# Optimization experiments

Measured on AMD Instinct MI355X. Metric: run time of the kernel, lower is better.

The kernel has to match this reference:

```python
import math
import jax, jax.numpy as jnp
import numpy as np

B, Q, K, D = 32, 1024, 1024, 128
MASK_VALUE = -1000000.0


def setup_inputs() -> dict:
    key = jax.random.key(0)
    kq, kk, kv, kl = jax.random.split(key, 4)
    return {
        "queries": jax.random.normal(kq, (B, Q, D), dtype=jnp.float32),
        "keys": jax.random.normal(kk, (B, K, D), dtype=jnp.float32),
        "values": jax.random.normal(kv, (B, K, D), dtype=jnp.float32),
        "valid_lens": jax.random.randint(kl, (B,), 1, K + 1, dtype=jnp.int32),
    }


def reference(queries, keys, values, valid_lens):
    d = queries.shape[-1]
    # scores: [B, Q, K]
    scores = jnp.einsum("bqd,bkd->bqk", queries, keys) / math.sqrt(d)
    # key-padding mask: position k valid iff k < valid_lens[b] (broadcast over queries)
    mask = jnp.arange(keys.shape[1])[None, None, :] < valid_lens[:, None, None]
    scores = jnp.where(mask, scores, MASK_VALUE)
    attn = jax.nn.softmax(scores, axis=-1)
    # dropout p=0.0 -> identity
    return jnp.einsum("bqk,bkv->bqv", attn, values)
```

## Files before the change

kernel.cpp:

```cpp
#include <hip/hip_runtime.h>
#include <math.h>

typedef _Float16 f16;
typedef __attribute__((ext_vector_type(8))) _Float16 f16x8;
typedef __attribute__((ext_vector_type(4))) _Float16 f16x4;
typedef __attribute__((ext_vector_type(4))) float f32x4;

constexpr int BATCH = 32;
constexpr int QL = 1024;
constexpr int KL = 1024;
constexpr int D = 128;
constexpr int BQ = 64;
constexpr int BK = 64;
constexpr int CT = 8;
constexpr int DKP = 136;
constexpr int BKP = 72;

#define CSC 0.12752863187087177f

static __device__ __forceinline__ f16x4 pk4(float x, float y, float z, float w) {
  auto a = __builtin_amdgcn_cvt_pkrtz(x, y);
  auto b = __builtin_amdgcn_cvt_pkrtz(z, w);
  f16x4 h;
  h[0] = (f16)a[0]; h[1] = (f16)a[1]; h[2] = (f16)b[0]; h[3] = (f16)b[1];
  return h;
}
static __device__ __forceinline__ f16x8 pk8(float4 u, float4 v) {
  f16x4 a = pk4(u.x, u.y, u.z, u.w);
  f16x4 b = pk4(v.x, v.y, v.z, v.w);
  f16x8 h;
  h[0] = a[0]; h[1] = a[1]; h[2] = a[2]; h[3] = a[3];
  h[4] = b[0]; h[5] = b[1]; h[6] = b[2]; h[7] = b[3];
  return h;
}
static __device__ __forceinline__ f16x8 pk8v(f32x4 a, f32x4 b) {
  auto x0 = __builtin_amdgcn_cvt_pkrtz(a[0], a[1]);
  auto x1 = __builtin_amdgcn_cvt_pkrtz(a[2], a[3]);
  auto x2 = __builtin_amdgcn_cvt_pkrtz(b[0], b[1]);
  auto x3 = __builtin_amdgcn_cvt_pkrtz(b[2], b[3]);
  f16x8 h;
  h[0] = x0[0]; h[1] = x0[1]; h[2] = x1[0]; h[3] = x1[1];
  h[4] = x2[0]; h[5] = x2[1]; h[6] = x3[0]; h[7] = x3[1];
  return h;
}
static __device__ __forceinline__ f16x8 pk8s(float4 u, float4 v) {
  float4 a = {u.x * CSC, u.y * CSC, u.z * CSC, u.w * CSC};
  float4 b = {v.x * CSC, v.y * CSC, v.z * CSC, v.w * CSC};
  return pk8(a, b);
}

static __device__ __forceinline__ int krp(int kk) {
  return ((kk >> 5) << 5) | (((kk >> 2) & 1) << 4) | (((kk >> 3) & 3) << 2) | (kk & 3);
}

#define ISSUE(KR, VR, T)                                                   \
  do {                                                                     \
    const float4* Kt = (const float4*)(Kb + (size_t)(T) * BK * D);         \
    _Pragma("unroll")                                                      \
    for (int i_ = 0; i_ < 4; ++i_) {                                       \
      int cc_ = tid + i_ * 256;                                            \
      int row_ = cc_ >> 4, d04_ = (cc_ & 15) * 2;                          \
      KR[2 * i_]     = Kt[row_ * 32 + d04_];                               \
      KR[2 * i_ + 1] = Kt[row_ * 32 + d04_ + 1];                           \
    }                                                                      \
    const float* Vt = Vb + (size_t)(T) * BK * D;                           \
    _Pragma("unroll")                                                      \
    for (int i_ = 0; i_ < 2; ++i_) {                                       \
      int f_ = tid + i_ * 256;                                             \
      const float* base_ = Vt + (size_t)((f_ & 15) * 4) * D + (f_ >> 4) * 4; \
      VR[i_ * 4 + 0] = *(const float4*)(base_);                            \
      VR[i_ * 4 + 1] = *(const float4*)(base_ + D);                        \
      VR[i_ * 4 + 2] = *(const float4*)(base_ + 2 * D);                    \
      VR[i_ * 4 + 3] = *(const float4*)(base_ + 3 * D);                    \
    }                                                                      \
  } while (0)

#define DRAIN(KR, VR, NB)                                                  \
  do {                                                                     \
    _Pragma("unroll")                                                      \
    for (int i_ = 0; i_ < 4; ++i_) {                                       \
      int cc_ = tid + i_ * 256;                                            \
      int row_ = cc_ >> 4, d0_ = (cc_ & 15) * 8;                           \
      *(f16x8*)&sK[NB][krp(row_)][d0_] = pk8(KR[2 * i_], KR[2 * i_ + 1]);  \
    }                                                                      \
    _Pragma("unroll")                                                      \
    for (int i_ = 0; i_ < 2; ++i_) {                                       \
      int f_ = tid + i_ * 256;                                             \
      int k0_ = (f_ & 15) * 4, d0_ = (f_ >> 4) * 4;                        \
      float4 r0_ = VR[i_*4+0], r1_ = VR[i_*4+1], r2_ = VR[i_*4+2], r3_ = VR[i_*4+3]; \
      *(f16x4*)&sVT[NB][d0_ + 0][k0_] = pk4(r0_.x, r1_.x, r2_.x, r3_.x);   \
      *(f16x4*)&sVT[NB][d0_ + 1][k0_] = pk4(r0_.y, r1_.y, r2_.y, r3_.y);   \
      *(f16x4*)&sVT[NB][d0_ + 2][k0_] = pk4(r0_.z, r1_.z, r2_.z, r3_.z);   \
      *(f16x4*)&sVT[NB][d0_ + 3][k0_] = pk4(r0_.w, r1_.w, r2_.w, r3_.w);   \
    }                                                                      \
  } while (0)

#define TILE_BARRIER()                                                     \
  do {                                                                     \
    asm volatile("s_waitcnt lgkmcnt(0)" ::: "memory");                     \
    __builtin_amdgcn_s_barrier();                                          \
    asm volatile("" ::: "memory");                                         \
  } while (0)

__global__ __launch_bounds__(256, 2)
void attn_fwd(const float* __restrict__ Qp, const float* __restrict__ Kp,
              const float* __restrict__ Vp, const int* __restrict__ VLp,
              float* __restrict__ Op, float* __restrict__ wsO,
              float* __restrict__ wsL, int nks) {
  __shared__ f16 sK[2][BK][DKP];
  __shared__ f16 sVT[2][D][BKP];
  __shared__ int sN[32];
  __shared__ int sI[32];

  const int tid  = threadIdx.x;
  const int wave = tid >> 6, lane = tid & 63;
  const int l16  = lane & 15, quad = lane >> 4;

  if (tid < 32) sN[tid] = (VLp[tid] + BK - 1) / BK;
  __syncthreads();
  if (tid < 32) {
    int nb = sN[tid], r = 0;
    #pragma unroll
    for (int k = 0; k < 32; ++k) {
      int nk = sN[k];
      r += (nk > nb) || (nk == nb && k < tid);
    }
    sI[r] = tid;
  }
  __syncthreads();

  const int xcd = blockIdx.x & 7;
  const int j   = (int)blockIdx.x >> 3;

  int b, qt, ks, t0, t1, nt, vl;
  if (nks == 2) {
    ks = j >> 6;
    const int lb = (j >> 4) & 3;
    qt = j & 15;
    const int gr = (lb == 0) ? xcd : (lb == 1) ? (15 - xcd)
                 : (lb == 2) ? (16 + xcd) : (31 - xcd);
    b  = sI[gr];
    vl = VLp[b];
    nt = (vl + BK - 1) / BK;
    t0 = ks * CT;
    t1 = min(nt, t0 + CT);
    if (t0 >= t1) return;
  } else {
    const int jj = (j < 32) ? j : (95 - j);
    const int lr = jj >> 4;
    qt = jj & 15;
    ks = 0;
    const int gr = (lr == 0) ? xcd : (lr == 1) ? (15 - xcd)
                 : (lr == 2) ? (16 + xcd) : (31 - xcd);
    b  = sI[gr];
    vl = VLp[b];
    nt = (vl + BK - 1) / BK;
    t0 = 0; t1 = nt;
  }

  const float* Kb = Kp + (size_t)b * KL * D;
  const float* Vb = Vp + (size_t)b * KL * D;

  float4 kreg[8], vreg[8];

  const float* Qb = Qp + ((size_t)(b * QL + qt * BQ + wave * 16 + l16)) * D;
  float4 qtmp[8];
  #pragma unroll
  for (int kc = 0; kc < 4; ++kc) {
    const float* p = Qb + kc * 32 + quad * 8;
    qtmp[2 * kc]     = *(const float4*)p;
    qtmp[2 * kc + 1] = *(const float4*)(p + 4);
  }

  ISSUE(kreg, vreg, t0);

  f16x8 qf[4];
  #pragma unroll
  for (int kc = 0; kc < 4; ++kc) qf[kc] = pk8s(qtmp[2 * kc], qtmp[2 * kc + 1]);

  float lsum = 0.f;
  f32x4 o[8];
  #pragma unroll
  for (int dt = 0; dt < 8; ++dt) o[dt] = (f32x4){0.f, 0.f, 0.f, 0.f};

  DRAIN(kreg, vreg, 0);
  TILE_BARRIER();

  for (int t = t0; t < t1; ++t) {
    const int cur = (t - t0) & 1, nxt = cur ^ 1;
    const bool more = (t + 1 < t1);

    if (more) ISSUE(kreg, vreg, t + 1);

    f32x4 sv[4];
    #pragma unroll
    for (int ct = 0; ct < 4; ++ct) {
      f32x4 cacc = (f32x4){0.f, 0.f, 0.f, 0.f};
      #pragma unroll
      for (int kc = 0; kc < 4; ++kc) {
        f16x8 kf = *(const f16x8*)&sK[cur][ct * 16 + l16][kc * 32 + quad * 8];
        cacc = __builtin_amdgcn_mfma_f32_16x16x32_f16(kf, qf[kc], cacc, 0, 0, 0);
      }
      sv[ct] = cacc;
    }

    if (t * BK + BK > vl) {
      #pragma unroll
      for (int ct = 0; ct < 4; ++ct) {
        int kb = t * BK + (ct >> 1) * 32 + (ct & 1) * 4 + quad * 8;
        #pragma unroll
        for (int r = 0; r < 4; ++r)
          sv[ct][r] = (kb + r) < vl ? sv[ct][r] : -1.0e9f;
      }
    }

    #pragma unroll
    for (int ct = 0; ct < 4; ++ct) {
      #pragma unroll
      for (int r = 0; r < 4; ++r) {
        float p = __builtin_amdgcn_exp2f(sv[ct][r]);
        sv[ct][r] = p;
        lsum += p;
      }
    }
    f16x8 pf0 = pk8v(sv[0], sv[1]);
    f16x8 pf1 = pk8v(sv[2], sv[3]);

    #pragma unroll
    for (int dt = 0; dt < 8; ++dt) {
      f16x8 vf0 = *(const f16x8*)&sVT[cur][dt * 16 + l16][quad * 8];
      o[dt] = __builtin_amdgcn_mfma_f32_16x16x32_f16(vf0, pf0, o[dt], 0, 0, 0);
      f16x8 vf1 = *(const f16x8*)&sVT[cur][dt * 16 + l16][32 + quad * 8];
      o[dt] = __builtin_amdgcn_mfma_f32_16x16x32_f16(vf1, pf1, o[dt], 0, 0, 0);
    }

    if (more) DRAIN(kreg, vreg, nxt);
    TILE_BARRIER();
  }

  float ls = lsum;
  ls += __shfl_xor(ls, 16);
  ls += __shfl_xor(ls, 32);

  if (nks == 1 || nt <= CT) {
    float* Ob = Op + ((size_t)(b * QL + qt * BQ + wave * 16)) * D;
    const float inv = 1.0f / ls;
    #pragma unroll
    for (int dt = 0; dt < 8; ++dt) {
      float4 w = {o[dt][0] * inv, o[dt][1] * inv, o[dt][2] * inv, o[dt][3] * inv};
      *(float4*)&Ob[(size_t)l16 * D + dt * 16 + quad * 4] = w;
    }
  } else {
    const int pair = b * 16 + qt;
    float* dst = (ks == 0)
        ? Op + ((size_t)(b * QL + qt * BQ + wave * 16)) * D
        : wsO + (size_t)pair * BQ * D + (size_t)(wave * 16) * D;
    #pragma unroll
    for (int dt = 0; dt < 8; ++dt) {
      float4 w = {o[dt][0], o[dt][1], o[dt][2], o[dt][3]};
      *(float4*)&dst[(size_t)l16 * D + dt * 16 + quad * 4] = w;
    }
    if (quad == 0) wsL[(pair * 2 + ks) * 64 + wave * 16 + l16] = ls;
  }
}

__global__ __launch_bounds__(256)
void attn_combine(float* __restrict__ Op, const float* __restrict__ wsO,
                  const float* __restrict__ wsL, const int* __restrict__ VLp) {
  const int pair = blockIdx.x;
  const int b = pair >> 4;
  if (VLp[b] <= CT * BK) return;
  float* Ob = Op + ((size_t)(b * QL + (pair & 15) * BQ)) * D;
  const float* o1 = wsO + (size_t)pair * BQ * D;
  const float* Lt = wsL + pair * 128;
  const int tid = threadIdx.x;
  #pragma unroll
  for (int i = 0; i < 8; ++i) {
    int fi = tid + i * 256;
    int row = fi >> 5;
    float inv = 1.0f / (Lt[row] + Lt[64 + row]);
    float4 a = ((const float4*)Ob)[fi];
    float4 c = ((const float4*)o1)[fi];
    float4 w = {(a.x + c.x) * inv, (a.y + c.y) * inv,
                (a.z + c.z) * inv, (a.w + c.w) * inv};
    ((float4*)Ob)[fi] = w;
  }
}

extern "C" void kernel_launch(void* const* d_in, const int* in_sizes, int n_in,
                              void* d_out, int out_size, void* d_ws, size_t ws_size,
                              hipStream_t stream) {
  const float* Qp = (const float*)d_in[0];
  const float* Kp = (const float*)d_in[1];
  const float* Vp = (const float*)d_in[2];
  const int*   VL = (const int*)d_in[3];
  float* Op = (float*)d_out;

  const size_t n_pairs = (size_t)BATCH * (QL / BQ);
  const size_t need = n_pairs * BQ * D * 4 + n_pairs * 128 * 4;
  if (d_ws != nullptr && ws_size >= need) {
    float* wsO = (float*)d_ws;
    float* wsL = (float*)d_ws + n_pairs * BQ * D;
    attn_fwd<<<dim3(2 * (int)n_pairs), dim3(256), 0, stream>>>(
        Qp, Kp, Vp, VL, Op, wsO, wsL, 2);
    attn_combine<<<dim3((int)n_pairs), dim3(256), 0, stream>>>(Op, wsO, wsL, VL);
  } else {
    attn_fwd<<<dim3((int)n_pairs), dim3(256), 0, stream>>>(
        Qp, Kp, Vp, VL, Op, nullptr, nullptr, 1);
  }
}
```

Baseline: 127.2 us.

## Double query tile per block so each wave reuses K/V fragments across two row groups

Raises the query tile from 64 to 128 rows, with each wave now handling 32 query rows as two 16-row MFMA groups that share every K and V fragment loaded from LDS. This halves the K/V global loads and LDS reads per query row, and the block-to-batch schedule and split-K combine indexing are reworked to match. The cost is twice as many accumulator registers, which may reduce occupancy, and half as many blocks, which weakens load balancing across CUs for the variable-length batches.

After: 118.5 us. 1.07x faster.

```diff
diff --git a/kernel.cpp b/kernel.cpp
--- a/kernel.cpp
+++ b/kernel.cpp
@@ -10,7 +10,7 @@
 constexpr int QL = 1024;
 constexpr int KL = 1024;
 constexpr int D = 128;
-constexpr int BQ = 64;
+constexpr int BQ = 128;
 constexpr int BK = 64;
 constexpr int CT = 8;
 constexpr int DKP = 136;
@@ -130,13 +130,12 @@
   __syncthreads();
 
   const int xcd = blockIdx.x & 7;
-  const int j   = (int)blockIdx.x >> 3;
-
-  int b, qt, ks, t0, t1, nt, vl;
+  const int i   = (int)blockIdx.x >> 3;
+
+  int b, qt, ks, lb, t0, t1, nt, vl;
   if (nks == 2) {
-    ks = j >> 6;
-    const int lb = (j >> 4) & 3;
-    qt = j & 15;
+    if (i < 32) { ks = 0; lb = i >> 3;              qt = i & 7; }
+    else        { ks = 1; lb = 3 - ((i - 32) >> 3); qt = (i - 32) & 7; }
     const int gr = (lb == 0) ? xcd : (lb == 1) ? (15 - xcd)
                  : (lb == 2) ? (16 + xcd) : (31 - xcd);
     b  = sI[gr];
@@ -146,12 +145,9 @@
     t1 = min(nt, t0 + CT);
     if (t0 >= t1) return;
   } else {
-    const int jj = (j < 32) ? j : (95 - j);
-    const int lr = jj >> 4;
-    qt = jj & 15;
-    ks = 0;
-    const int gr = (lr == 0) ? xcd : (lr == 1) ? (15 - xcd)
-                 : (lr == 2) ? (16 + xcd) : (31 - xcd);
+    ks = 0; lb = i >> 3; qt = i & 7;
+    const int gr = (lb == 0) ? xcd : (lb == 1) ? (15 - xcd)
+                 : (lb == 2) ? (16 + xcd) : (31 - xcd);
     b  = sI[gr];
     vl = VLp[b];
     nt = (vl + BK - 1) / BK;
@@ -163,25 +159,34 @@
 
   float4 kreg[8], vreg[8];
 
-  const float* Qb = Qp + ((size_t)(b * QL + qt * BQ + wave * 16 + l16)) * D;
-  float4 qtmp[8];
-  #pragma unroll
-  for (int kc = 0; kc < 4; ++kc) {
-    const float* p = Qb + kc * 32 + quad * 8;
-    qtmp[2 * kc]     = *(const float4*)p;
-    qtmp[2 * kc + 1] = *(const float4*)(p + 4);
-  }
+  const float* Qb = Qp + ((size_t)(b * QL + qt * BQ + wave * 32 + l16)) * D;
+  float4 qtmp[16];
+  #pragma unroll
+  for (int h = 0; h < 2; ++h)
+    #pragma unroll
+    for (int kc = 0; kc < 4; ++kc) {
+      const float* p = Qb + h * 16 * D + kc * 32 + quad * 8;
+      qtmp[h * 8 + 2 * kc]     = *(const float4*)p;
+      qtmp[h * 8 + 2 * kc + 1] = *(const float4*)(p + 4);
+    }
 
   ISSUE(kreg, vreg, t0);
 
-  f16x8 qf[4];
-  #pragma unroll
-  for (int kc = 0; kc < 4; ++kc) qf[kc] = pk8s(qtmp[2 * kc], qtmp[2 * kc + 1]);
-
-  float lsum = 0.f;
-  f32x4 o[8];
-  #pragma unroll
-  for (int dt = 0; dt < 8; ++dt) o[dt] = (f32x4){0.f, 0.f, 0.f, 0.f};
+  f16x8 qf0[4], qf1[4];
+  #pragma unroll
+  for (int kc = 0; kc < 4; ++kc)
+    qf0[kc] = pk8s(qtmp[2 * kc], qtmp[2 * kc + 1]);
+  #pragma unroll
+  for (int kc = 0; kc < 4; ++kc)
+    qf1[kc] = pk8s(qtmp[8 + 2 * kc], qtmp[8 + 2 * kc + 1]);
+
+  float ls0 = 0.f, ls1 = 0.f;
+  f32x4 o0[8], o1[8];
+  #pragma unroll
+  for (int dt = 0; dt < 8; ++dt) {
+    o0[dt] = (f32x4){0.f, 0.f, 0.f, 0.f};
+    o1[dt] = (f32x4){0.f, 0.f, 0.f, 0.f};
+  }
 
   DRAIN(kreg, vreg, 0);
   TILE_BARRIER();
@@ -192,16 +197,17 @@
 
     if (more) ISSUE(kreg, vreg, t + 1);
 
-    f32x4 sv[4];
+    f32x4 s0[4], s1[4];
     #pragma unroll
     for (int ct = 0; ct < 4; ++ct) {
-      f32x4 cacc = (f32x4){0.f, 0.f, 0.f, 0.f};
+      s0[ct] = (f32x4){0.f, 0.f, 0.f, 0.f};
+      s1[ct] = (f32x4){0.f, 0.f, 0.f, 0.f};
       #pragma unroll
       for (int kc = 0; kc < 4; ++kc) {
         f16x8 kf = *(const f16x8*)&sK[cur][ct * 16 + l16][kc * 32 + quad * 8];
-        cacc = __builtin_amdgcn_mfma_f32_16x16x32_f16(kf, qf[kc], cacc, 0, 0, 0);
+        s0[ct] = __builtin_amdgcn_mfma_f32_16x16x32_f16(kf, qf0[kc], s0[ct], 0, 0, 0);
+        s1[ct] = __builtin_amdgcn_mfma_f32_16x16x32_f16(kf, qf1[kc], s1[ct], 0, 0, 0);
       }
-      sv[ct] = cacc;
     }
 
     if (t * BK + BK > vl) {
@@ -209,8 +215,11 @@
       for (int ct = 0; ct < 4; ++ct) {
         int kb = t * BK + (ct >> 1) * 32 + (ct & 1) * 4 + quad * 8;
         #pragma unroll
-        for (int r = 0; r < 4; ++r)
-          sv[ct][r] = (kb + r) < vl ? sv[ct][r] : -1.0e9f;
+        for (int r = 0; r < 4; ++r) {
+          bool ok = (kb + r) < vl;
+          s0[ct][r] = ok ? s0[ct][r] : -1.0e9f;
+          s1[ct][r] = ok ? s1[ct][r] : -1.0e9f;
+        }
       }
     }
 
@@ -218,49 +227,61 @@
     for (int ct = 0; ct < 4; ++ct) {
       #pragma unroll
       for (int r = 0; r < 4; ++r) {
-        float p = __builtin_amdgcn_exp2f(sv[ct][r]);
-        sv[ct][r] = p;
-        lsum += p;
+        float p0 = __builtin_amdgcn_exp2f(s0[ct][r]);
+        float p1 = __builtin_amdgcn_exp2f(s1[ct][r]);
+        s0[ct][r] = p0; ls0 += p0;
+        s1[ct][r] = p1; ls1 += p1;
       }
     }
-    f16x8 pf0 = pk8v(sv[0], sv[1]);
-    f16x8 pf1 = pk8v(sv[2], sv[3]);
+    f16x8 pa0 = pk8v(s0[0], s0[1]), pb0 = pk8v(s0[2], s0[3]);
+    f16x8 pa1 = pk8v(s1[0], s1[1]), pb1 = pk8v(s1[2], s1[3]);
 
     #pragma unroll
     for (int dt = 0; dt < 8; ++dt) {
       f16x8 vf0 = *(const f16x8*)&sVT[cur][dt * 16 + l16][quad * 8];
-      o[dt] = __builtin_amdgcn_mfma_f32_16x16x32_f16(vf0, pf0, o[dt], 0, 0, 0);
+      o0[dt] = __builtin_amdgcn_mfma_f32_16x16x32_f16(vf0, pa0, o0[dt], 0, 0, 0);
+      o1[dt] = __builtin_amdgcn_mfma_f32_16x16x32_f16(vf0, pa1, o1[dt], 0, 0, 0);
       f16x8 vf1 = *(const f16x8*)&sVT[cur][dt * 16 + l16][32 + quad * 8];
-      o[dt] = __builtin_amdgcn_mfma_f32_16x16x32_f16(vf1, pf1, o[dt], 0, 0, 0);
+      o0[dt] = __builtin_amdgcn_mfma_f32_16x16x32_f16(vf1, pb0, o0[dt], 0, 0, 0);
+      o1[dt] = __builtin_amdgcn_mfma_f32_16x16x32_f16(vf1, pb1, o1[dt], 0, 0, 0);
     }
 
     if (more) DRAIN(kreg, vreg, nxt);
     TILE_BARRIER();
   }
 
-  float ls = lsum;
-  ls += __shfl_xor(ls, 16);
-  ls += __shfl_xor(ls, 32);
-
+  ls0 += __shfl_xor(ls0, 16);
+  ls0 += __shfl_xor(ls0, 32);
+  ls1 += __shfl_xor(ls1, 16);
+  ls1 += __shfl_xor(ls1, 32);
+
+  const int row0 = qt * BQ + wave * 32;
   if (nks == 1 || nt <= CT) {
-    float* Ob = Op + ((size_t)(b * QL + qt * BQ + wave * 16)) * D;
-    const float inv = 1.0f / ls;
+    float* Ob = Op + ((size_t)(b * QL + row0)) * D;
+    const float i0 = 1.0f / ls0, i1 = 1.0f / ls1;
     #pragma unroll
     for (int dt = 0; dt < 8; ++dt) {
-      float4 w = {o[dt][0] * inv, o[dt][1] * inv, o[dt][2] * inv, o[dt][3] * inv};
-      *(float4*)&Ob[(size_t)l16 * D + dt * 16 + quad * 4] = w;
+      float4 w0 = {o0[dt][0] * i0, o0[dt][1] * i0, o0[dt][2] * i0, o0[dt][3] * i0};
+      float4 w1 = {o1[dt][0] * i1, o1[dt][1] * i1, o1[dt][2] * i1, o1[dt][3] * i1};
+      *(float4*)&Ob[(size_t)l16 * D + dt * 16 + quad * 4]        = w0;
+      *(float4*)&Ob[(size_t)(16 + l16) * D + dt * 16 + quad * 4] = w1;
     }
   } else {
-    const int pair = b * 16 + qt;
+    const int pair = b * 8 + qt;
     float* dst = (ks == 0)
-        ? Op + ((size_t)(b * QL + qt * BQ + wave * 16)) * D
-        : wsO + (size_t)pair * BQ * D + (size_t)(wave * 16) * D;
+        ? Op + ((size_t)(b * QL + row0)) * D
+        : wsO + (size_t)pair * BQ * D + (size_t)(wave * 32) * D;
     #pragma unroll
     for (int dt = 0; dt < 8; ++dt) {
-      float4 w = {o[dt][0], o[dt][1], o[dt][2], o[dt][3]};
-      *(float4*)&dst[(size_t)l16 * D + dt * 16 + quad * 4] = w;
-    }
-    if (quad == 0) wsL[(pair * 2 + ks) * 64 + wave * 16 + l16] = ls;
+      float4 w0 = {o0[dt][0], o0[dt][1], o0[dt][2], o0[dt][3]};
+      float4 w1 = {o1[dt][0], o1[dt][1], o1[dt][2], o1[dt][3]};
+      *(float4*)&dst[(size_t)l16 * D + dt * 16 + quad * 4]        = w0;
+      *(float4*)&dst[(size_t)(16 + l16) * D + dt * 16 + quad * 4] = w1;
+    }
+    if (quad == 0) {
+      wsL[(pair * 2 + ks) * 128 + wave * 32 + l16]      = ls0;
+      wsL[(pair * 2 + ks) * 128 + wave * 32 + 16 + l16] = ls1;
+    }
   }
 }
 
@@ -268,19 +289,19 @@
 void attn_combine(float* __restrict__ Op, const float* __restrict__ wsO,
                   const float* __restrict__ wsL, const int* __restrict__ VLp) {
   const int pair = blockIdx.x;
-  const int b = pair >> 4;
+  const int b = pair >> 3;
   if (VLp[b] <= CT * BK) return;
-  float* Ob = Op + ((size_t)(b * QL + (pair & 15) * BQ)) * D;
-  const float* o1 = wsO + (size_t)pair * BQ * D;
-  const float* Lt = wsL + pair * 128;
+  float* Ob = Op + ((size_t)(b * QL + (pair & 7) * BQ)) * D;
+  const float4* o1 = (const float4*)(wsO + (size_t)pair * BQ * D);
+  const float* Lt = wsL + (size_t)pair * 256;
   const int tid = threadIdx.x;
   #pragma unroll
-  for (int i = 0; i < 8; ++i) {
+  for (int i = 0; i < 16; ++i) {
     int fi = tid + i * 256;
     int row = fi >> 5;
-    float inv = 1.0f / (Lt[row] + Lt[64 + row]);
+    float inv = 1.0f / (Lt[row] + Lt[128 + row]);
     float4 a = ((const float4*)Ob)[fi];
-    float4 c = ((const float4*)o1)[fi];
+    float4 c = o1[fi];
     float4 w = {(a.x + c.x) * inv, (a.y + c.y) * inv,
                 (a.z + c.z) * inv, (a.w + c.w) * inv};
     ((float4*)Ob)[fi] = w;
@@ -297,7 +318,7 @@
   float* Op = (float*)d_out;
 
   const size_t n_pairs = (size_t)BATCH * (QL / BQ);
-  const size_t need = n_pairs * BQ * D * 4 + n_pairs * 128 * 4;
+  const size_t need = n_pairs * BQ * D * 4 + n_pairs * 256 * 4;
   if (d_ws != nullptr && ws_size >= need) {
     float* wsO = (float*)d_ws;
     float* wsL = (float*)d_ws + n_pairs * BQ * D;
```
